# Kernel tuning notes

Measured on AMD Instinct MI355X. Metric: run time of the kernel, lower is better.

The kernel has to match this reference:

```python
import jax, jax.numpy as jnp
import numpy as np


def setup_inputs() -> dict:
    key = jax.random.key(0)
    k_x, k_idx, k_sgn = jax.random.split(key, 3)
    batch, original_dim, proj_dim, c = 32, 1000000, 4096, 8
    x = jax.random.normal(k_x, (batch, original_dim), dtype=jnp.float32)
    rand_indices = jax.random.randint(k_idx, (original_dim, c), 0, proj_dim, dtype=jnp.int32)
    # random signs in {-1, +1}, matching torch.randint(0,2)*2-1 cast to int8
    rand_signs = (jax.random.randint(k_sgn, (original_dim, c), 0, 2, dtype=jnp.int32) * 2 - 1)
    return {"x": x, "rand_indices": rand_indices, "rand_signs": rand_signs,
            "proj_dim": proj_dim, "c": c}


def reference(x, rand_indices, rand_signs, proj_dim, c):
    # SJLT: each input coordinate d is scattered to c random output buckets
    # with random sign; normalized by 1/sqrt(c) so the sketch preserves norms.
    scale = jnp.asarray(1.0 / np.sqrt(c), dtype=x.dtype)
    batch = x.shape[0]
    out = jnp.zeros((batch, proj_dim), dtype=x.dtype)
    # c is a small fixed constant; loop over it, vectorize over batch & features.
    for j in range(c):
        vals = x * rand_signs[:, j].astype(x.dtype)      # [B, D]
        out = out.at[:, rand_indices[:, j]].add(vals)     # scatter-add along proj dim
    return out * scale
```

## Files before the change

kernel.cpp:

```cpp
#include <hip/hip_runtime.h>
#include <hip/hip_fp16.h>


#define D_TOTAL 1000000
#define PROJ    4096
#define C_SK    8
#define NE      (D_TOTAL * C_SK)
#define SCALE   0.35355339059327373f

#define NSEG    16
#define SEG_D   62500
#define CAPA2   8448
#define BINCAP_A 96
#define CAPH    96
#define TILE    4096
#define NBLK_A  ((NE + TILE - 1) / TILE)
#define NBLK_T  ((D_TOTAL + 255) / 256)
#define NSLICE  (NSEG * 2)

#define SMEM_A  25088

#define CURA_OFF   0
#define XT_OFF     16384
#define XT_SZ      ((size_t)D_TOTAL * 32 * 2)
#define LISTA_OFF  (XT_OFF + XT_SZ)
#define LISTA_SZ   ((size_t)NSEG * 64 * CAPA2 * 4)
#define PART_OFF   (LISTA_OFF + LISTA_SZ)
#define PART_SZ    ((size_t)NSLICE * PROJ * 32 * 4)
#define WS_NEED    (PART_OFF + PART_SZ)

__global__ void init_cursors_kernel(int* __restrict__ curA) {
    int i = blockIdx.x * blockDim.x + threadIdx.x;
    if (i < NSEG * 64) curA[i] = i * CAPA2;
}

template<int BC>
__device__ __forceinline__ void rank_and_stage(bool ok, int kb, int payload,
                                               int* __restrict__ cnt,
                                               int* __restrict__ stage,
                                               int* __restrict__ gcur,
                                               int* __restrict__ glist,
                                               int gcur_idx, int glim) {
    if (ok) {
        const int pos = atomicAdd(&cnt[kb], 1);
        if (pos < BC) {
            stage[kb * BC + pos] = payload;
        } else {
            const int gp = atomicAdd(&gcur[gcur_idx], 1);
            if (gp < glim) glist[gp] = payload;
        }
    }
}

template<int BC>
__device__ __forceinline__ void flush_bins(int* __restrict__ cnt,
                                           int* __restrict__ basek,
                                           const int* __restrict__ stage,
                                           int* __restrict__ gcur,
                                           int* __restrict__ glist,
                                           int gidx0, int capPer) {
    const int tid = threadIdx.x;
    if (tid < 64) {
        const int m = min(cnt[tid], BC);
        cnt[tid]   = m;
        basek[tid] = atomicAdd(&gcur[gidx0 + tid], m);
    }
    __syncthreads();
    const int w = tid >> 6, lane = tid & 63;
    #pragma unroll 1
    for (int bi = 0; bi < 16; ++bi) {
        const int kb  = w * 16 + bi;
        const int m   = cnt[kb];
        const int gb  = basek[kb];
        const int lim = (gidx0 + kb + 1) * capPer;
        for (int i = lane; i < m; i += 64)
            if (gb + i < lim) glist[gb + i] = stage[kb * BC + i];
    }
}

__device__ __forceinline__ void pass_a_body(int abid, char* smem,
                                            const int* __restrict__ idx,
                                            const int* __restrict__ sgn,
                                            int* __restrict__ curA,
                                            int* __restrict__ listA) {
    int* stage = (int*)smem;
    int* cnt   = (int*)(smem + 64 * BINCAP_A * 4);
    int* basek = cnt + 64;
    const int tid = threadIdx.x;
    if (tid < 64) cnt[tid] = 0;
    __syncthreads();

    const int d_lo = abid * 512;
    const int seg  = d_lo / SEG_D;
    const bool boundary = ((d_lo + 511) / SEG_D) != seg;
    const int v0 = abid * (TILE / 4);

    #pragma unroll 1
    for (int k = 0; k < TILE / 1024; ++k) {
        const int vi = v0 + k * 256 + tid;
        const bool okv = vi < NE / 4;
        int4 i4 = {0,0,0,0}, s4 = {0,0,0,0};
        if (okv) { i4 = ((const int4*)idx)[vi]; s4 = ((const int4*)sgn)[vi]; }
        const int g0 = vi * 4;
        #pragma unroll
        for (int m = 0; m < 4; ++m) {
            const int bucket = (m == 0) ? i4.x : (m == 1) ? i4.y : (m == 2) ? i4.z : i4.w;
            const int sg     = (m == 0) ? s4.x : (m == 1) ? s4.y : (m == 2) ? s4.z : s4.w;
            const int kb = okv ? (bucket >> 6) : 0;
            const int payload = (g0 + m) | ((bucket & 63) << 24)
                              | (int)((unsigned)sg & 0x80000000u);
            if (!boundary) {
                rank_and_stage<BINCAP_A>(okv, kb, payload, cnt, stage, curA, listA,
                                         seg * 64 + kb, (seg * 64 + kb + 1) * CAPA2);
            } else if (okv) {
                const int segE = ((g0 + m) >> 3) / SEG_D;
                const int bin  = segE * 64 + kb;
                const int gp = atomicAdd(&curA[bin], 1);
                if (gp < (bin + 1) * CAPA2) listA[gp] = payload;
            }
        }
    }
    __syncthreads();
    flush_bins<BINCAP_A>(cnt, basek, stage, curA, listA, seg * 64, CAPA2);
}

__global__ __launch_bounds__(256, 6)
void pass_a_kernel(const int* __restrict__ idx, const int* __restrict__ sgn,
                   int* __restrict__ curA, int* __restrict__ listA) {
    __shared__ char smem[SMEM_A];
    pass_a_body(blockIdx.x, smem, idx, sgn, curA, listA);
}

__global__ __launch_bounds__(256, 8)
void transpose_kernel(const float* __restrict__ x, unsigned short* __restrict__ xT) {
    __shared__ __align__(16) unsigned short tile[256 * 36];
    const int tid = threadIdx.x;
    const int d0  = blockIdx.x * 256;
    const int o   = tid & 3;
    const int dq  = tid >> 2;
    const int dbase = d0 + dq * 4;

    float4 v[8];
    if (dbase + 4 <= D_TOTAL) {
        #pragma unroll
        for (int j = 0; j < 8; ++j)
            v[j] = *(const float4*)(x + (size_t)(o * 8 + j) * D_TOTAL + dbase);
    } else {
        #pragma unroll
        for (int j = 0; j < 8; ++j) {
            v[j].x = v[j].y = v[j].z = v[j].w = 0.f;
            const float* row = x + (size_t)(o * 8 + j) * D_TOTAL;
            if (dbase + 0 < D_TOTAL) v[j].x = row[dbase + 0];
            if (dbase + 1 < D_TOTAL) v[j].y = row[dbase + 1];
            if (dbase + 2 < D_TOTAL) v[j].z = row[dbase + 2];
            if (dbase + 3 < D_TOTAL) v[j].w = row[dbase + 3];
        }
    }

    const int s = dq & 7;
    #pragma unroll
    for (int m = 0; m < 4; ++m) {
        unsigned short h[8];
        #pragma unroll
        for (int j = 0; j < 8; ++j) {
            const float f = (m == 0) ? v[j].x : (m == 1) ? v[j].y
                          : (m == 2) ? v[j].z : v[j].w;
            h[j] = __half_as_ushort(__float2half(f));
        }
        const int row = dq * 4 + m;
        unsigned short* rbase = &tile[row * 36];
        *(uint2*)(rbase + (((2 * o + 0) ^ s) << 2)) = *(const uint2*)&h[0];
        *(uint2*)(rbase + (((2 * o + 1) ^ s) << 2)) = *(const uint2*)&h[4];
    }
    __syncthreads();

    #pragma unroll
    for (int k = 0; k < 4; ++k) {
        const int dl = k * 64 + (tid >> 2);
        if (d0 + dl < D_TOTAL) {
            const int s2 = (dl >> 2) & 7;
            const unsigned short* rbase = &tile[dl * 36];
            const uint2 r0 = *(const uint2*)(rbase + (((2 * o + 0) ^ s2) << 2));
            const uint2 r1 = *(const uint2*)(rbase + (((2 * o + 1) ^ s2) << 2));
            uint4 w; w.x = r0.x; w.y = r0.y; w.z = r1.x; w.w = r1.y;
            *(uint4*)(xT + (size_t)(d0 + dl) * 32 + o * 8) = w;
        }
    }
}

__global__ __launch_bounds__(256, 6)
void gather_part_kernel(const int* __restrict__ curA, const int* __restrict__ listA,
                        const unsigned short* __restrict__ xT,
                        float* __restrict__ partial, float* __restrict__ out) {
    __shared__ int stage[64 * CAPH];
    __shared__ int cnt[64];
    const int tid = threadIdx.x;
    const int gid = blockIdx.x;
    const int seg  = (gid & 7) + 8 * (gid >> 10);
    const int rest = (gid >> 3) & 127;
    const int kbA  = rest >> 1;
    const int half = rest & 1;
    const int part = seg * 64 + kbA;

    if (tid < 64) cnt[tid] = 0;
    __syncthreads();

    const int pstart = part * CAPA2;
    const int pcount = min(curA[part] - pstart, CAPA2);
    const int hn = (pcount + 1) >> 1;
    const int t0 = half * hn;
    const int t1 = min(t0 + hn, pcount);

    for (int i = t0 + tid; i < t1; i += 256) {
        const int e  = listA[pstart + i];
        const int kb = (e >> 24) & 63;
        const int pos = atomicAdd(&cnt[kb], 1);
        if (pos < CAPH) {
            stage[kb * CAPH + pos] = e;
        } else {
            int d = (e & 0x7FFFFF) >> 3;
            d = min(d, D_TOTAL - 1);
            const float sgf = (e < 0) ? -SCALE : SCALE;
            const int p = kbA * 64 + kb;
            for (int b = 0; b < 32; ++b) {
                const float vv = __half2float(*(const __half*)(xT + (size_t)d * 32 + b));
                unsafeAtomicAdd(out + (size_t)b * PROJ + p, sgf * vv);
            }
        }
    }
    __syncthreads();

    const int w    = tid >> 6;
    const int lane = tid & 63;
    const int slot = lane >> 2;
    const int bq   = lane & 3;
    #pragma unroll 1
    for (int bi = 0; bi < 16; ++bi) {
        const int kb = w * 16 + bi;
        const int n  = min(cnt[kb], CAPH);
        float a0=0.f,a1=0.f,a2=0.f,a3=0.f,a4=0.f,a5=0.f,a6=0.f,a7=0.f;
        #pragma unroll 2
        for (int base = 0; base < n; base += 16) {
            const int  e  = base + slot;
            const bool ok = e < n;
            const int  pl = stage[kb * CAPH + (ok ? e : 0)];
            int d = (pl & 0x7FFFFF) >> 3;
            d = min(d, D_TOTAL - 1);
            const float sg = ok ? ((pl < 0) ? -1.f : 1.f) : 0.f;
            const uint4 hv = *(const uint4*)(xT + (size_t)d * 32 + bq * 8);
            float2 f;
            f = __half22float2(*(const __half2*)&hv.x); a0 = fmaf(sg, f.x, a0); a1 = fmaf(sg, f.y, a1);
            f = __half22float2(*(const __half2*)&hv.y); a2 = fmaf(sg, f.x, a2); a3 = fmaf(sg, f.y, a3);
            f = __half22float2(*(const __half2*)&hv.z); a4 = fmaf(sg, f.x, a4); a5 = fmaf(sg, f.y, a5);
            f = __half22float2(*(const __half2*)&hv.w); a6 = fmaf(sg, f.x, a6); a7 = fmaf(sg, f.y, a7);
        }
        #pragma unroll
        for (int m = 4; m <= 32; m <<= 1) {
            a0 += __shfl_xor(a0, m, 64); a1 += __shfl_xor(a1, m, 64);
            a2 += __shfl_xor(a2, m, 64); a3 += __shfl_xor(a3, m, 64);
            a4 += __shfl_xor(a4, m, 64); a5 += __shfl_xor(a5, m, 64);
            a6 += __shfl_xor(a6, m, 64); a7 += __shfl_xor(a7, m, 64);
        }
        if (lane < 4) {
            float vv[8] = {a0,a1,a2,a3,a4,a5,a6,a7};
            const size_t slice = (size_t)(seg * 2 + half);
            float* dst = partial + (slice * PROJ + (size_t)(kbA * 64 + kb)) * 32 + lane * 8;
            #pragma unroll
            for (int i = 0; i < 8; ++i) dst[i] = vv[i];
        }
    }
}

__global__ __launch_bounds__(256)
void reduce_kernel(const float* __restrict__ partial, float* __restrict__ out) {
    const int gtid = blockIdx.x * 256 + threadIdx.x;
    const int p = gtid & (PROJ - 1);
    const int b = gtid >> 12;
    float s = 0.f;
    #pragma unroll
    for (int sg = 0; sg < NSLICE; ++sg)
        s += partial[((size_t)(sg * PROJ + p)) * 32 + b];
    const size_t oidx = (size_t)b * PROJ + p;
    out[oidx] = out[oidx] + s * SCALE;
}

#define BG 8
#define NCHUNK 64
#define BLOCK 1024
__global__ __launch_bounds__(BLOCK, 4)
void sjlt_scatter_fallback(const float* __restrict__ x,
                           const int* __restrict__ idx,
                           const int* __restrict__ sgn,
                           float* __restrict__ out) {
    __shared__ float acc[BG * PROJ];
    const int tid = threadIdx.x;
    #pragma unroll
    for (int i = 0; i < (BG * PROJ) / BLOCK; ++i) acc[i * BLOCK + tid] = 0.0f;
    __syncthreads();
    const int chunk = D_TOTAL / NCHUNK;
    const int d0 = blockIdx.x * chunk;
    const int d1 = d0 + chunk;
    const int bg = blockIdx.y * BG;
    for (int d = d0 + tid; d < d1; d += BLOCK) {
        const int4 i0 = *(const int4*)(idx + (size_t)d * C_SK);
        const int4 i1 = *(const int4*)(idx + (size_t)d * C_SK + 4);
        const int4 s0 = *(const int4*)(sgn + (size_t)d * C_SK);
        const int4 s1 = *(const int4*)(sgn + (size_t)d * C_SK + 4);
        #pragma unroll
        for (int b = 0; b < BG; ++b) {
            const float xv = __builtin_nontemporal_load(x + (size_t)(bg + b) * D_TOTAL + d);
            const unsigned xb = __float_as_uint(xv);
            float* accb = acc + b * PROJ;
            atomicAdd(accb + i0.x, __uint_as_float(xb ^ ((unsigned)s0.x & 0x80000000u)));
            atomicAdd(accb + i0.y, __uint_as_float(xb ^ ((unsigned)s0.y & 0x80000000u)));
            atomicAdd(accb + i0.z, __uint_as_float(xb ^ ((unsigned)s0.z & 0x80000000u)));
            atomicAdd(accb + i0.w, __uint_as_float(xb ^ ((unsigned)s0.w & 0x80000000u)));
            atomicAdd(accb + i1.x, __uint_as_float(xb ^ ((unsigned)s1.x & 0x80000000u)));
            atomicAdd(accb + i1.y, __uint_as_float(xb ^ ((unsigned)s1.y & 0x80000000u)));
            atomicAdd(accb + i1.z, __uint_as_float(xb ^ ((unsigned)s1.z & 0x80000000u)));
            atomicAdd(accb + i1.w, __uint_as_float(xb ^ ((unsigned)s1.w & 0x80000000u)));
        }
    }
    __syncthreads();
    #pragma unroll
    for (int i = 0; i < (BG * PROJ) / BLOCK; ++i) {
        const int lin = i * BLOCK + tid;
        const int b = lin >> 12;
        const int pp = lin & (PROJ - 1);
        unsafeAtomicAdd(out + (size_t)(bg + b) * PROJ + pp, acc[lin] * SCALE);
    }
}

extern "C" void kernel_launch(void* const* d_in, const int* in_sizes, int n_in,
                              void* d_out, int out_size, void* d_ws, size_t ws_size,
                              hipStream_t stream) {
    const float* x   = (const float*)d_in[0];
    const int*   idx = (const int*)d_in[1];
    const int*   sgn = (const int*)d_in[2];
    float*       out = (float*)d_out;

    if (ws_size < WS_NEED) {
        (void)hipMemsetAsync(out, 0, (size_t)out_size * sizeof(float), stream);
        dim3 grid(NCHUNK, 32 / BG);
        sjlt_scatter_fallback<<<grid, BLOCK, 0, stream>>>(x, idx, sgn, out);
        return;
    }

    char* ws = (char*)d_ws;
    int*            curA    = (int*)(ws + CURA_OFF);
    unsigned short* xT      = (unsigned short*)(ws + XT_OFF);
    int*            listA   = (int*)(ws + LISTA_OFF);
    float*          partial = (float*)(ws + PART_OFF);

    (void)hipMemsetAsync(out, 0, (size_t)out_size * sizeof(float), stream);
    init_cursors_kernel<<<4, 256, 0, stream>>>(curA);
    pass_a_kernel<<<NBLK_A, 256, 0, stream>>>(idx, sgn, curA, listA);
    transpose_kernel<<<NBLK_T, 256, 0, stream>>>(x, xT);
    gather_part_kernel<<<2048, 256, 0, stream>>>(curA, listA, xT, partial, out);
    reduce_kernel<<<(32 * PROJ) / 256, 256, 0, stream>>>(partial, out);
}
```

Baseline: 367.3 us.

## Add nontemporal loads/stores, dual-accumulator gather, and vectorized reduce

Marks streaming global traffic (index/sign reads, x reads, xT writes, list writes, partial writes and reads) as nontemporal so it does not pollute the cache. The gather loop handles two entries per iteration with separate accumulators, giving more independent xT loads in flight. The reduce kernel is restructured so each thread reads float4 partials contiguously, with fewer blocks. The risk is that nontemporal hints push out data that later kernels would reuse from L2/MALL, such as xT in the gather step, and the reduce now writes out with strided, less coalesced stores.

```diff
diff --git a/kernel.cpp b/kernel.cpp
--- a/kernel.cpp
+++ b/kernel.cpp
@@ -17,6 +17,15 @@
 #define NBLK_A  ((NE + TILE - 1) / TILE)
 #define NBLK_T  ((D_TOTAL + 255) / 256)
 #define NSLICE  (NSEG * 2)
+
+typedef int          ni4 __attribute__((ext_vector_type(4)));
+typedef float        nf4 __attribute__((ext_vector_type(4)));
+typedef unsigned int nu4 __attribute__((ext_vector_type(4)));
+
+__device__ __forceinline__ float2 h2f2(unsigned int u) {
+    union { unsigned int u; __half2 h; } cv; cv.u = u;
+    return __half22float2(cv.h);
+}
 
 #define SMEM_A  25088
 
@@ -74,7 +83,8 @@
         const int gb  = basek[kb];
         const int lim = (gidx0 + kb + 1) * capPer;
         for (int i = lane; i < m; i += 64)
-            if (gb + i < lim) glist[gb + i] = stage[kb * BC + i];
+            if (gb + i < lim)
+                __builtin_nontemporal_store(stage[kb * BC + i], &glist[gb + i]);
     }
 }
 
@@ -99,13 +109,16 @@
     for (int k = 0; k < TILE / 1024; ++k) {
         const int vi = v0 + k * 256 + tid;
         const bool okv = vi < NE / 4;
-        int4 i4 = {0,0,0,0}, s4 = {0,0,0,0};
-        if (okv) { i4 = ((const int4*)idx)[vi]; s4 = ((const int4*)sgn)[vi]; }
+        ni4 i4 = {0,0,0,0}, s4 = {0,0,0,0};
+        if (okv) {
+            i4 = __builtin_nontemporal_load(&((const ni4*)idx)[vi]);
+            s4 = __builtin_nontemporal_load(&((const ni4*)sgn)[vi]);
+        }
         const int g0 = vi * 4;
         #pragma unroll
         for (int m = 0; m < 4; ++m) {
-            const int bucket = (m == 0) ? i4.x : (m == 1) ? i4.y : (m == 2) ? i4.z : i4.w;
-            const int sg     = (m == 0) ? s4.x : (m == 1) ? s4.y : (m == 2) ? s4.z : s4.w;
+            const int bucket = i4[m];
+            const int sg     = s4[m];
             const int kb = okv ? (bucket >> 6) : 0;
             const int payload = (g0 + m) | ((bucket & 63) << 24)
                               | (int)((unsigned)sg & 0x80000000u);
@@ -140,20 +153,21 @@
     const int dq  = tid >> 2;
     const int dbase = d0 + dq * 4;
 
-    float4 v[8];
+    nf4 v[8];
     if (dbase + 4 <= D_TOTAL) {
         #pragma unroll
         for (int j = 0; j < 8; ++j)
-            v[j] = *(const float4*)(x + (size_t)(o * 8 + j) * D_TOTAL + dbase);
+            v[j] = __builtin_nontemporal_load(
+                (const nf4*)(x + (size_t)(o * 8 + j) * D_TOTAL + dbase));
     } else {
         #pragma unroll
         for (int j = 0; j < 8; ++j) {
-            v[j].x = v[j].y = v[j].z = v[j].w = 0.f;
+            v[j] = (nf4){0.f, 0.f, 0.f, 0.f};
             const float* row = x + (size_t)(o * 8 + j) * D_TOTAL;
-            if (dbase + 0 < D_TOTAL) v[j].x = row[dbase + 0];
-            if (dbase + 1 < D_TOTAL) v[j].y = row[dbase + 1];
-            if (dbase + 2 < D_TOTAL) v[j].z = row[dbase + 2];
-            if (dbase + 3 < D_TOTAL) v[j].w = row[dbase + 3];
+            if (dbase + 0 < D_TOTAL) v[j][0] = row[dbase + 0];
+            if (dbase + 1 < D_TOTAL) v[j][1] = row[dbase + 1];
+            if (dbase + 2 < D_TOTAL) v[j][2] = row[dbase + 2];
+            if (dbase + 3 < D_TOTAL) v[j][3] = row[dbase + 3];
         }
     }
 
@@ -162,11 +176,8 @@
     for (int m = 0; m < 4; ++m) {
         unsigned short h[8];
         #pragma unroll
-        for (int j = 0; j < 8; ++j) {
-            const float f = (m == 0) ? v[j].x : (m == 1) ? v[j].y
-                          : (m == 2) ? v[j].z : v[j].w;
-            h[j] = __half_as_ushort(__float2half(f));
-        }
+        for (int j = 0; j < 8; ++j)
+            h[j] = __half_as_ushort(__float2half(v[j][m]));
         const int row = dq * 4 + m;
         unsigned short* rbase = &tile[row * 36];
         *(uint2*)(rbase + (((2 * o + 0) ^ s) << 2)) = *(const uint2*)&h[0];
@@ -182,8 +193,9 @@
             const unsigned short* rbase = &tile[dl * 36];
             const uint2 r0 = *(const uint2*)(rbase + (((2 * o + 0) ^ s2) << 2));
             const uint2 r1 = *(const uint2*)(rbase + (((2 * o + 1) ^ s2) << 2));
-            uint4 w; w.x = r0.x; w.y = r0.y; w.z = r1.x; w.w = r1.y;
-            *(uint4*)(xT + (size_t)(d0 + dl) * 32 + o * 8) = w;
+            nu4 w; w[0] = r0.x; w[1] = r0.y; w[2] = r1.x; w[3] = r1.y;
+            __builtin_nontemporal_store(
+                w, (nu4*)(xT + (size_t)(d0 + dl) * 32 + o * 8));
         }
     }
 }
@@ -212,7 +224,7 @@
     const int t1 = min(t0 + hn, pcount);
 
     for (int i = t0 + tid; i < t1; i += 256) {
-        const int e  = listA[pstart + i];
+        const int e  = __builtin_nontemporal_load(&listA[pstart + i]);
         const int kb = (e >> 24) & 63;
         const int pos = atomicAdd(&cnt[kb], 1);
         if (pos < CAPH) {
@@ -239,21 +251,33 @@
         const int kb = w * 16 + bi;
         const int n  = min(cnt[kb], CAPH);
         float a0=0.f,a1=0.f,a2=0.f,a3=0.f,a4=0.f,a5=0.f,a6=0.f,a7=0.f;
+        float c0=0.f,c1=0.f,c2=0.f,c3=0.f,c4=0.f,c5=0.f,c6=0.f,c7=0.f;
         #pragma unroll 2
-        for (int base = 0; base < n; base += 16) {
-            const int  e  = base + slot;
-            const bool ok = e < n;
-            const int  pl = stage[kb * CAPH + (ok ? e : 0)];
-            int d = (pl & 0x7FFFFF) >> 3;
-            d = min(d, D_TOTAL - 1);
-            const float sg = ok ? ((pl < 0) ? -1.f : 1.f) : 0.f;
-            const uint4 hv = *(const uint4*)(xT + (size_t)d * 32 + bq * 8);
+        for (int base = 0; base < n; base += 32) {
+            const int  e0  = base + slot;
+            const int  e1  = base + 16 + slot;
+            const bool ok0 = e0 < n;
+            const bool ok1 = e1 < n;
+            const int  pl0 = stage[kb * CAPH + (ok0 ? e0 : 0)];
+            const int  pl1 = stage[kb * CAPH + (ok1 ? e1 : 0)];
+            int d0 = (pl0 & 0x7FFFFF) >> 3;  d0 = min(d0, D_TOTAL - 1);
+            int d1 = (pl1 & 0x7FFFFF) >> 3;  d1 = min(d1, D_TOTAL - 1);
+            const float s0 = ok0 ? ((pl0 < 0) ? -1.f : 1.f) : 0.f;
+            const float s1 = ok1 ? ((pl1 < 0) ? -1.f : 1.f) : 0.f;
+            const nu4 hv0 = *(const nu4*)(xT + (size_t)d0 * 32 + bq * 8);
+            const nu4 hv1 = *(const nu4*)(xT + (size_t)d1 * 32 + bq * 8);
             float2 f;
-            f = __half22float2(*(const __half2*)&hv.x); a0 = fmaf(sg, f.x, a0); a1 = fmaf(sg, f.y, a1);
-            f = __half22float2(*(const __half2*)&hv.y); a2 = fmaf(sg, f.x, a2); a3 = fmaf(sg, f.y, a3);
-            f = __half22float2(*(const __half2*)&hv.z); a4 = fmaf(sg, f.x, a4); a5 = fmaf(sg, f.y, a5);
-            f = __half22float2(*(const __half2*)&hv.w); a6 = fmaf(sg, f.x, a6); a7 = fmaf(sg, f.y, a7);
-        }
+            f = h2f2(hv0[0]); a0 = fmaf(s0, f.x, a0); a1 = fmaf(s0, f.y, a1);
+            f = h2f2(hv0[1]); a2 = fmaf(s0, f.x, a2); a3 = fmaf(s0, f.y, a3);
+            f = h2f2(hv0[2]); a4 = fmaf(s0, f.x, a4); a5 = fmaf(s0, f.y, a5);
+            f = h2f2(hv0[3]); a6 = fmaf(s0, f.x, a6); a7 = fmaf(s0, f.y, a7);
+            f = h2f2(hv1[0]); c0 = fmaf(s1, f.x, c0); c1 = fmaf(s1, f.y, c1);
+            f = h2f2(hv1[1]); c2 = fmaf(s1, f.x, c2); c3 = fmaf(s1, f.y, c3);
+            f = h2f2(hv1[2]); c4 = fmaf(s1, f.x, c4); c5 = fmaf(s1, f.y, c5);
+            f = h2f2(hv1[3]); c6 = fmaf(s1, f.x, c6); c7 = fmaf(s1, f.y, c7);
+        }
+        a0 += c0; a1 += c1; a2 += c2; a3 += c3;
+        a4 += c4; a5 += c5; a6 += c6; a7 += c7;
         #pragma unroll
         for (int m = 4; m <= 32; m <<= 1) {
             a0 += __shfl_xor(a0, m, 64); a1 += __shfl_xor(a1, m, 64);
@@ -262,26 +286,35 @@
             a6 += __shfl_xor(a6, m, 64); a7 += __shfl_xor(a7, m, 64);
         }
         if (lane < 4) {
-            float vv[8] = {a0,a1,a2,a3,a4,a5,a6,a7};
             const size_t slice = (size_t)(seg * 2 + half);
             float* dst = partial + (slice * PROJ + (size_t)(kbA * 64 + kb)) * 32 + lane * 8;
-            #pragma unroll
-            for (int i = 0; i < 8; ++i) dst[i] = vv[i];
+            nf4 v0 = {a0, a1, a2, a3};
+            nf4 v1 = {a4, a5, a6, a7};
+            __builtin_nontemporal_store(v0, (nf4*)dst);
+            __builtin_nontemporal_store(v1, (nf4*)(dst + 4));
         }
     }
 }
 
 __global__ __launch_bounds__(256)
 void reduce_kernel(const float* __restrict__ partial, float* __restrict__ out) {
-    const int gtid = blockIdx.x * 256 + threadIdx.x;
-    const int p = gtid & (PROJ - 1);
-    const int b = gtid >> 12;
-    float s = 0.f;
-    #pragma unroll
-    for (int sg = 0; sg < NSLICE; ++sg)
-        s += partial[((size_t)(sg * PROJ + p)) * 32 + b];
-    const size_t oidx = (size_t)b * PROJ + p;
-    out[oidx] = out[oidx] + s * SCALE;
+    const int tid = threadIdx.x;
+    const int bq  = tid & 7;
+    const int pl  = tid >> 3;
+    const int p   = blockIdx.x * 32 + pl;
+    nf4 s = {0.f, 0.f, 0.f, 0.f};
+    #pragma unroll
+    for (int sg = 0; sg < NSLICE; ++sg) {
+        const nf4 v = __builtin_nontemporal_load(
+            (const nf4*)(partial + ((size_t)sg * PROJ + p) * 32 + bq * 4));
+        s[0] += v[0]; s[1] += v[1]; s[2] += v[2]; s[3] += v[3];
+    }
+    #pragma unroll
+    for (int i = 0; i < 4; ++i) {
+        const int b = bq * 4 + i;
+        const size_t o = (size_t)b * PROJ + p;
+        out[o] = out[o] + s[i] * SCALE;
+    }
 }
 
 #define BG 8
@@ -357,5 +390,5 @@
     pass_a_kernel<<<NBLK_A, 256, 0, stream>>>(idx, sgn, curA, listA);
     transpose_kernel<<<NBLK_T, 256, 0, stream>>>(x, xT);
     gather_part_kernel<<<2048, 256, 0, stream>>>(curA, listA, xT, partial, out);
-    reduce_kernel<<<(32 * PROJ) / 256, 256, 0, stream>>>(partial, out);
-}
+    reduce_kernel<<<PROJ / 32, 256, 0, stream>>>(partial, out);
+}
```

Result: faster. 350.3 us (-4.6%).
